# Kernel optimization log

Measured on AMD Instinct MI355X. Metric: run time of the kernel, lower is better.

Reference implementation:

```python
import jax, jax.numpy as jnp
import numpy as np

IM_H, IM_W = 128, 128       # im_size
HT_H, HT_W = 184, 180       # ht_size (rho x theta)
N_VOTES = 4_000_000         # number of (pixel, bin, weight) vote triples
NORM = float(max(IM_H, IM_W))


def setup_inputs() -> dict:
    key = jax.random.key(0)
    k1, k2, k3, k4 = jax.random.split(key, 4)
    x = jax.random.normal(k1, (2, 16, IM_H, IM_W), dtype=jnp.float32)
    vote_pixel = jax.random.randint(k2, (N_VOTES,), 0, IM_H * IM_W)   # pixel flat index
    vote_bin = jax.random.randint(k3, (N_VOTES,), 0, HT_H * HT_W)     # HT bin flat index
    vote_weight = jax.random.uniform(k4, (N_VOTES,), dtype=jnp.float32)
    return {"x": x, "vote_pixel": vote_pixel, "vote_bin": vote_bin,
            "vote_weight": vote_weight}


def reference(x, vote_pixel, vote_bin, vote_weight):
    # The original view(b*2, c//2, r, w) is a pure reshape; the scatter is
    # independent per (batch, channel) map, so we flatten all maps together.
    b, c, r, w = x.shape
    xf = x.reshape(b * c, r * w)                         # [BC, P]
    gathered = xf[:, vote_pixel] * vote_weight[None, :]  # [BC, N]
    # weighted scatter-add into HT bins (segment sum over leading axis)
    out = jax.ops.segment_sum(gathered.T, vote_bin, num_segments=HT_H * HT_W)  # [HB, BC]
    out = out.T.reshape(b, c, HT_H, HT_W)
    return out / NORM
```

## Files before the change

kernel.cpp:

```cpp
#include <hip/hip_runtime.h>
#include <stdint.h>

#define IM_HW   16384
#define NBINS   33120
#define NMAPS   32
#define INV_NORM (1.0f / 128.0f)

#define BBITS   5
#define NBUCK   1035
#define CAPB    4352
#define SLAB    192
#define SSTR    194
#define NB_SCAT 256
#define OVR_CAP 8192

__device__ __forceinline__ float w_from_top13(unsigned e) {
  const unsigned short hb = (unsigned short)((e >> 19) << 3);
  return (float)__builtin_bit_cast(_Float16, hb);
}
__device__ __forceinline__ float f16u(unsigned short h) {
  return (float)__builtin_bit_cast(_Float16, h);
}

__global__ __launch_bounds__(1024) void k_scatter_bucket(
    const float* __restrict__ x, unsigned short* __restrict__ xT2,
    const int* __restrict__ vp, const int* __restrict__ vb,
    const float* __restrict__ vw, int nv,
    unsigned* __restrict__ globcur,
    unsigned* __restrict__ ovrcnt,
    uint2*   __restrict__ ovrlist,
    unsigned* __restrict__ sorted) {
  __shared__ unsigned h[NBUCK];
  __shared__ unsigned lstart[NBUCK];
  __shared__ unsigned cur[NBUCK];
  __shared__ unsigned lds[16384];

  const int tid = threadIdx.x;

  {
    const int base = blockIdx.x * 2048;
    #pragma unroll
    for (int k = 0; k < 2; ++k) {
      const int i = base + k * 1024 + tid;
      const int m = i & 31, p = i >> 5;
      xT2[i] = __builtin_bit_cast(unsigned short, (_Float16)x[m * IM_HW + p]);
    }
  }

  const int chunk = (((nv + NB_SCAT - 1) / NB_SCAT) + 3) & ~3;
  const int c0 = blockIdx.x * chunk;
  const int c1 = min(nv, c0 + chunk);
  const int cnt = (c1 > c0) ? (c1 - c0) : 0;

  for (int i = tid; i < NBUCK; i += 1024) h[i] = 0u;
  __syncthreads();

  unsigned e[16];
  unsigned short rr[16], bu16[16];
  const int ng = cnt >> 2;
  const int4*   vp4 = (const int4*)(vp + c0);
  const int4*   vb4 = (const int4*)(vb + c0);
  const float4* vw4 = (const float4*)(vw + c0);
  #pragma unroll
  for (int j = 0; j < 4; ++j) {
    const int g = tid + j * 1024;
    if (g < ng) {
      const int4 p = vp4[g]; const int4 b = vb4[g]; const float4 w = vw4[g];
      const int k = j * 4;
      #define STAGE(q, PP, BB, WW) { \
        const unsigned short hw = __builtin_bit_cast(unsigned short, (_Float16)(WW)); \
        e[k + q] = (unsigned)(PP) | (((unsigned)(BB) & 31u) << 14) | (((unsigned)hw >> 3) << 19); \
        bu16[k + q] = (unsigned short)((unsigned)(BB) >> BBITS); \
        rr[k + q] = (unsigned short)atomicAdd(&h[(unsigned)(BB) >> BBITS], 1u); }
      STAGE(0, p.x, b.x, w.x) STAGE(1, p.y, b.y, w.y)
      STAGE(2, p.z, b.z, w.z) STAGE(3, p.w, b.w, w.w)
      #undef STAGE
    }
  }
  const int tail0 = ng * 4;
  if (tid < cnt - tail0) {
    const int gi = c0 + tail0 + tid;
    unsigned o = atomicAdd(ovrcnt, 1u);
    if (o < OVR_CAP)
      ovrlist[o] = make_uint2((unsigned)vp[gi] | ((unsigned)vb[gi] << 14),
                              __float_as_uint(vw[gi]));
  }
  __syncthreads();

  if (tid < 64) {
    const int lo = tid * 17, hi = min(NBUCK, lo + 17);
    unsigned s = 0;
    for (int i = lo; i < hi; ++i) s += h[i];
    unsigned inc = s;
    #pragma unroll
    for (int d = 1; d < 64; d <<= 1) {
      const unsigned v = __shfl_up(inc, d);
      if (tid >= d) inc += v;
    }
    unsigned run = inc - s;
    for (int i = lo; i < hi; ++i) { lstart[i] = run; run += h[i]; }
  }
  __syncthreads();
  for (int i = tid; i < NBUCK; i += 1024)
    cur[i] = (h[i] != 0u) ? atomicAdd(&globcur[i], h[i]) : 0u;
  __syncthreads();

  #pragma unroll
  for (int j = 0; j < 4; ++j) {
    const int g = tid + j * 1024;
    if (g < ng) {
      #pragma unroll
      for (int q = 0; q < 4; ++q) {
        const int k = j * 4 + q;
        lds[lstart[bu16[k]] + (unsigned)rr[k]] = e[k];
      }
    }
  }
  __syncthreads();

  const int wid = tid >> 6, lane = tid & 63;
  for (int bu = wid; bu < NBUCK; bu += 16) {
    const unsigned c = h[bu];
    if (c == 0u) continue;
    const unsigned gb = cur[bu], lb = lstart[bu];
    for (unsigned s = lane; s < c; s += 64) {
      const unsigned E = lds[lb + s];
      const unsigned g = gb + s;
      if (g < CAPB) {
        sorted[(size_t)bu * CAPB + g] = E;
      } else {
        unsigned o = atomicAdd(ovrcnt, 1u);
        if (o < OVR_CAP) {
          const unsigned pp  = E & 0x3FFFu;
          const unsigned bin = ((unsigned)bu << BBITS) + ((E >> 14) & 31u);
          ovrlist[o] = make_uint2(pp | (bin << 14), __float_as_uint(w_from_top13(E)));
        }
      }
    }
  }
}

__global__ __launch_bounds__(512) void k_spmm_static(
    const unsigned* __restrict__ sorted, const unsigned* __restrict__ globcur,
    const unsigned short* __restrict__ xT2, float* __restrict__ out,
    unsigned* __restrict__ ovrcnt, uint2* __restrict__ ovrlist) {
  __shared__ unsigned sv[32 * SSTR];
  __shared__ unsigned cur[32];
  __shared__ float tile[32][33];
  const int tid = threadIdx.x;
  const int bu = blockIdx.x;
  const int n = min((int)globcur[bu], CAPB);

  if (tid < 32) cur[tid] = 0u;
  __syncthreads();

  const uint4* src = (const uint4*)(sorted + (size_t)bu * CAPB);
  const int nq = n >> 2;
  #define PLACE(E) { \
    const unsigned fb = ((E) >> 14) & 31u; \
    const unsigned s = atomicAdd(&cur[fb], 1u); \
    if (s < SLAB) sv[fb * SSTR + s] = (E) & 0xFFF83FFFu; \
    else { \
      unsigned o = atomicAdd(ovrcnt, 1u); \
      if (o < OVR_CAP) \
        ovrlist[o] = make_uint2(((E) & 0x3FFFu) | ((((unsigned)bu << BBITS) + fb) << 14), \
                                __float_as_uint(w_from_top13(E))); } }
  for (int i = tid; i < nq; i += 512) {
    const uint4 q = src[i];
    PLACE(q.x) PLACE(q.y) PLACE(q.z) PLACE(q.w)
  }
  if (tid < (n & 3)) {
    const unsigned E = sorted[(size_t)bu * CAPB + (n & ~3) + tid];
    PLACE(E)
  }
  #undef PLACE
  __syncthreads();

  #define WDEC(E) ((float)__builtin_bit_cast(_Float16, (unsigned short)((E) >> 16)))
  const unsigned* xh2 = (const unsigned*)xT2;
  const int wv = tid >> 6, lane = tid & 63;
  const int q = lane >> 4, mp = lane & 15;
  #pragma unroll
  for (int s4 = 0; s4 < 4; ++s4) {
    const int b = wv * 4 + s4;
    const int cnt = min((int)cur[b], SLAB);
    const unsigned* seg = &sv[b * SSTR];
    float acc0 = 0.0f, acc1 = 0.0f;
    int base = 0;
    for (; base + 8 <= cnt; base += 8) {
      const uint2 a = *(const uint2*)(seg + base + 2 * q);
      {
        const unsigned xv = xh2[(a.x & 0x3FFFu) * 16 + mp];
        const float w = WDEC(a.x);
        acc0 += w * f16u((unsigned short)(xv & 0xFFFFu));
        acc1 += w * f16u((unsigned short)(xv >> 16));
      }
      {
        const unsigned xv = xh2[(a.y & 0x3FFFu) * 16 + mp];
        const float w = WDEC(a.y);
        acc0 += w * f16u((unsigned short)(xv & 0xFFFFu));
        acc1 += w * f16u((unsigned short)(xv >> 16));
      }
    }
    for (int j = base + q; j < cnt; j += 4) {
      const unsigned E = seg[j];
      const unsigned xv = xh2[(E & 0x3FFFu) * 16 + mp];
      const float w = WDEC(E);
      acc0 += w * f16u((unsigned short)(xv & 0xFFFFu));
      acc1 += w * f16u((unsigned short)(xv >> 16));
    }
    acc0 += __shfl_xor(acc0, 16); acc0 += __shfl_xor(acc0, 32);
    acc1 += __shfl_xor(acc1, 16); acc1 += __shfl_xor(acc1, 32);
    if (lane < 16) {
      tile[b][2 * mp]     = acc0 * INV_NORM;
      tile[b][2 * mp + 1] = acc1 * INV_NORM;
    }
  }
  #undef WDEC
  __syncthreads();

  {
    unsigned nov = *ovrcnt;
    nov = nov < (unsigned)OVR_CAP ? nov : (unsigned)OVR_CAP;
    if (nov) {
      for (unsigned idx = tid; idx < nov * 32u; idx += 512u) {
        const unsigned vi = idx >> 5, m2 = idx & 31u;
        const uint2 vv = ovrlist[vi];
        const unsigned bin = vv.x >> 14;
        if ((bin >> BBITS) == (unsigned)bu) {
          const float xv = f16u(xT2[(vv.x & 0x3FFFu) * 32 + m2]);
          atomicAdd(&tile[bin & 31u][m2],
                    __uint_as_float(vv.y) * xv * INV_NORM);
        }
      }
      __syncthreads();
    }
  }

  {
    const int row  = tid >> 4;
    const int col2 = (tid & 15) * 2;
    const int gb0  = bu << BBITS;
    const float2 v2 = make_float2(tile[col2][row], tile[col2 + 1][row]);
    *(float2*)(out + (size_t)row * NBINS + gb0 + col2) = v2;
  }
}

__global__ __launch_bounds__(1024) void ht_fallback(const float* __restrict__ x,
                                                    const int* __restrict__ vp,
                                                    const int* __restrict__ vb,
                                                    const float* __restrict__ vw,
                                                    float* __restrict__ out, int nv) {
  __shared__ float hist[NBINS];
  for (int i = threadIdx.x; i < NBINS; i += 1024) hist[i] = 0.0f;
  __syncthreads();
  const int map = blockIdx.x >> 3, chunk = blockIdx.x & 7;
  const float* xm = x + map * IM_HW;
  const int per = (nv + 7) / 8;
  const int start = chunk * per, end = min(nv, start + per);
  for (int i = start + (int)threadIdx.x; i < end; i += 1024)
    atomicAdd(&hist[vb[i]], xm[vp[i]] * vw[i]);
  __syncthreads();
  float* om = out + map * NBINS;
  for (int i = threadIdx.x; i < NBINS; i += 1024)
    atomicAdd(&om[i], hist[i] * INV_NORM);
}

extern "C" void kernel_launch(void* const* d_in, const int* in_sizes, int n_in,
                              void* d_out, int out_size, void* d_ws, size_t ws_size,
                              hipStream_t stream) {
  const float* x  = (const float*)d_in[0];
  const int*   vp = (const int*)d_in[1];
  const int*   vb = (const int*)d_in[2];
  const float* vw = (const float*)d_in[3];
  float* out = (float*)d_out;
  const int nv = in_sizes[1];

  char* w = (char*)d_ws;
  unsigned*       sorted  = (unsigned*)w;       w += (size_t)NBUCK * CAPB * 4;
  unsigned short* xT2     = (unsigned short*)w; w += (size_t)IM_HW * NMAPS * 2;
  uint2*          ovrlist = (uint2*)w;          w += (size_t)OVR_CAP * 8;
  unsigned*       globcur = (unsigned*)w;       w += (size_t)NBUCK * 4;
  unsigned*       ovrcnt  = (unsigned*)w;       w += 16;
  const size_t need = (size_t)(w - (char*)d_ws);

  if (ws_size >= need) {
    hipMemsetAsync(globcur, 0, (size_t)NBUCK * 4 + 16, stream);
    k_scatter_bucket<<<NB_SCAT, 1024, 0, stream>>>(x, xT2, vp, vb, vw, nv, globcur,
                                                   ovrcnt, ovrlist, sorted);
    k_spmm_static<<<NBUCK, 512, 0, stream>>>(sorted, globcur, xT2, out,
                                             ovrcnt, ovrlist);
  } else {
    hipMemsetAsync(out, 0, (size_t)out_size * sizeof(float), stream);
    ht_fallback<<<256, 1024, 0, stream>>>(x, vp, vb, vw, out, nv);
  }
}
```

Measured before the change: 151.8 us.

## Use more smaller scatter blocks and wider 4-map gathers in SpMM

The bucketing kernel moves from 256 blocks of 1024 threads to 768 blocks of 512 threads, with a smaller LDS staging buffer. This should improve occupancy and spread the vote binning across more CUs. Only the first 512 blocks now transpose x, and the per-block vote chunk drops to about 5.2K votes, which fits the 5376-entry LDS buffer. The SpMM inner loop loads 8 bytes (4 fp16 maps) per lane instead of 4 bytes, with 8 votes in flight per wavefront instead of 4, which adds one extra shuffle stage to the reduction.

```diff
diff --git a/kernel.cpp b/kernel.cpp
--- a/kernel.cpp
+++ b/kernel.cpp
@@ -11,7 +11,9 @@
 #define CAPB    4352
 #define SLAB    192
 #define SSTR    194
-#define NB_SCAT 256
+#define NB_SCAT 768
+#define NT_SCAT 512
+#define LDSVOT  5376
 #define OVR_CAP 8192
 
 __device__ __forceinline__ float w_from_top13(unsigned e) {
@@ -22,7 +24,7 @@
   return (float)__builtin_bit_cast(_Float16, h);
 }
 
-__global__ __launch_bounds__(1024) void k_scatter_bucket(
+__global__ __launch_bounds__(NT_SCAT) void k_scatter_bucket(
     const float* __restrict__ x, unsigned short* __restrict__ xT2,
     const int* __restrict__ vp, const int* __restrict__ vb,
     const float* __restrict__ vw, int nv,
@@ -33,15 +35,15 @@
   __shared__ unsigned h[NBUCK];
   __shared__ unsigned lstart[NBUCK];
   __shared__ unsigned cur[NBUCK];
-  __shared__ unsigned lds[16384];
+  __shared__ unsigned lds[LDSVOT];
 
   const int tid = threadIdx.x;
 
-  {
-    const int base = blockIdx.x * 2048;
+  if (blockIdx.x < 512) {
+    const int base = blockIdx.x * 1024;
     #pragma unroll
     for (int k = 0; k < 2; ++k) {
-      const int i = base + k * 1024 + tid;
+      const int i = base + k * NT_SCAT + tid;
       const int m = i & 31, p = i >> 5;
       xT2[i] = __builtin_bit_cast(unsigned short, (_Float16)x[m * IM_HW + p]);
     }
@@ -52,7 +54,7 @@
   const int c1 = min(nv, c0 + chunk);
   const int cnt = (c1 > c0) ? (c1 - c0) : 0;
 
-  for (int i = tid; i < NBUCK; i += 1024) h[i] = 0u;
+  for (int i = tid; i < NBUCK; i += NT_SCAT) h[i] = 0u;
   __syncthreads();
 
   unsigned e[16];
@@ -63,7 +65,7 @@
   const float4* vw4 = (const float4*)(vw + c0);
   #pragma unroll
   for (int j = 0; j < 4; ++j) {
-    const int g = tid + j * 1024;
+    const int g = tid + j * NT_SCAT;
     if (g < ng) {
       const int4 p = vp4[g]; const int4 b = vb4[g]; const float4 w = vw4[g];
       const int k = j * 4;
@@ -101,13 +103,13 @@
     for (int i = lo; i < hi; ++i) { lstart[i] = run; run += h[i]; }
   }
   __syncthreads();
-  for (int i = tid; i < NBUCK; i += 1024)
+  for (int i = tid; i < NBUCK; i += NT_SCAT)
     cur[i] = (h[i] != 0u) ? atomicAdd(&globcur[i], h[i]) : 0u;
   __syncthreads();
 
   #pragma unroll
   for (int j = 0; j < 4; ++j) {
-    const int g = tid + j * 1024;
+    const int g = tid + j * NT_SCAT;
     if (g < ng) {
       #pragma unroll
       for (int q = 0; q < 4; ++q) {
@@ -119,7 +121,7 @@
   __syncthreads();
 
   const int wid = tid >> 6, lane = tid & 63;
-  for (int bu = wid; bu < NBUCK; bu += 16) {
+  for (int bu = wid; bu < NBUCK; bu += 8) {
     const unsigned c = h[bu];
     if (c == 0u) continue;
     const unsigned gb = cur[bu], lb = lstart[bu];
@@ -177,43 +179,53 @@
   __syncthreads();
 
   #define WDEC(E) ((float)__builtin_bit_cast(_Float16, (unsigned short)((E) >> 16)))
-  const unsigned* xh2 = (const unsigned*)xT2;
+  const uint2* xh4 = (const uint2*)xT2;
   const int wv = tid >> 6, lane = tid & 63;
-  const int q = lane >> 4, mp = lane & 15;
+  const int q = lane >> 3, mp = lane & 7;
   #pragma unroll
   for (int s4 = 0; s4 < 4; ++s4) {
     const int b = wv * 4 + s4;
     const int cnt = min((int)cur[b], SLAB);
     const unsigned* seg = &sv[b * SSTR];
-    float acc0 = 0.0f, acc1 = 0.0f;
+    float a0 = 0.0f, a1 = 0.0f, a2 = 0.0f, a3 = 0.0f;
     int base = 0;
-    for (; base + 8 <= cnt; base += 8) {
+    for (; base + 16 <= cnt; base += 16) {
       const uint2 a = *(const uint2*)(seg + base + 2 * q);
       {
-        const unsigned xv = xh2[(a.x & 0x3FFFu) * 16 + mp];
+        const uint2 xv = xh4[(a.x & 0x3FFFu) * 8 + mp];
         const float w = WDEC(a.x);
-        acc0 += w * f16u((unsigned short)(xv & 0xFFFFu));
-        acc1 += w * f16u((unsigned short)(xv >> 16));
+        a0 += w * f16u((unsigned short)(xv.x & 0xFFFFu));
+        a1 += w * f16u((unsigned short)(xv.x >> 16));
+        a2 += w * f16u((unsigned short)(xv.y & 0xFFFFu));
+        a3 += w * f16u((unsigned short)(xv.y >> 16));
       }
       {
-        const unsigned xv = xh2[(a.y & 0x3FFFu) * 16 + mp];
+        const uint2 xv = xh4[(a.y & 0x3FFFu) * 8 + mp];
         const float w = WDEC(a.y);
-        acc0 += w * f16u((unsigned short)(xv & 0xFFFFu));
-        acc1 += w * f16u((unsigned short)(xv >> 16));
-      }
-    }
-    for (int j = base + q; j < cnt; j += 4) {
+        a0 += w * f16u((unsigned short)(xv.x & 0xFFFFu));
+        a1 += w * f16u((unsigned short)(xv.x >> 16));
+        a2 += w * f16u((unsigned short)(xv.y & 0xFFFFu));
+        a3 += w * f16u((unsigned short)(xv.y >> 16));
+      }
+    }
+    for (int j = base + q; j < cnt; j += 8) {
       const unsigned E = seg[j];
-      const unsigned xv = xh2[(E & 0x3FFFu) * 16 + mp];
+      const uint2 xv = xh4[(E & 0x3FFFu) * 8 + mp];
       const float w = WDEC(E);
-      acc0 += w * f16u((unsigned short)(xv & 0xFFFFu));
-      acc1 += w * f16u((unsigned short)(xv >> 16));
-    }
-    acc0 += __shfl_xor(acc0, 16); acc0 += __shfl_xor(acc0, 32);
-    acc1 += __shfl_xor(acc1, 16); acc1 += __shfl_xor(acc1, 32);
-    if (lane < 16) {
-      tile[b][2 * mp]     = acc0 * INV_NORM;
-      tile[b][2 * mp + 1] = acc1 * INV_NORM;
+      a0 += w * f16u((unsigned short)(xv.x & 0xFFFFu));
+      a1 += w * f16u((unsigned short)(xv.x >> 16));
+      a2 += w * f16u((unsigned short)(xv.y & 0xFFFFu));
+      a3 += w * f16u((unsigned short)(xv.y >> 16));
+    }
+    a0 += __shfl_xor(a0, 8); a0 += __shfl_xor(a0, 16); a0 += __shfl_xor(a0, 32);
+    a1 += __shfl_xor(a1, 8); a1 += __shfl_xor(a1, 16); a1 += __shfl_xor(a1, 32);
+    a2 += __shfl_xor(a2, 8); a2 += __shfl_xor(a2, 16); a2 += __shfl_xor(a2, 32);
+    a3 += __shfl_xor(a3, 8); a3 += __shfl_xor(a3, 16); a3 += __shfl_xor(a3, 32);
+    if (lane < 8) {
+      tile[b][4 * mp]     = a0 * INV_NORM;
+      tile[b][4 * mp + 1] = a1 * INV_NORM;
+      tile[b][4 * mp + 2] = a2 * INV_NORM;
+      tile[b][4 * mp + 3] = a3 * INV_NORM;
     }
   }
   #undef WDEC
@@ -286,8 +298,8 @@
 
   if (ws_size >= need) {
     hipMemsetAsync(globcur, 0, (size_t)NBUCK * 4 + 16, stream);
-    k_scatter_bucket<<<NB_SCAT, 1024, 0, stream>>>(x, xT2, vp, vb, vw, nv, globcur,
-                                                   ovrcnt, ovrlist, sorted);
+    k_scatter_bucket<<<NB_SCAT, NT_SCAT, 0, stream>>>(x, xT2, vp, vb, vw, nv, globcur,
+                                                      ovrcnt, ovrlist, sorted);
     k_spmm_static<<<NBUCK, 512, 0, stream>>>(sorted, globcur, xT2, out,
                                              ovrcnt, ovrlist);
   } else {
```

After: 172.6 us. +13.7%, slower.
